# Kernel optimization log

Measured on AMD Instinct MI355X. Metric: run time of the kernel, lower is better.

The kernel has to match this reference:

```python
import jax, jax.numpy as jnp
import numpy as np

PAD = 4          # displacement radius
WIN = 2 * PAD + 1  # 9 -> 81 displacement channels


def setup_inputs() -> dict:
    key = jax.random.key(0)
    k1, k2 = jax.random.split(key)
    B, C, H, W = 4, 128, 128, 256
    first = jax.random.normal(k1, (B, C, H, W), dtype=jnp.float32)
    second = jax.random.normal(k2, (B, C, H, W), dtype=jnp.float32)
    return {"first": first, "second": second}


def reference(first, second):
    """FlowNet-style correlation / cost volume.

    out[b, (p+4)*9 + (o+4), y, x] = mean_c first[b,c,y,x] * second_pad[b,c,y+p+4,x+o+4]
    with second zero-padded by 4 on each spatial side.
    """
    B, C, H, W = first.shape
    second_pad = jnp.pad(second, ((0, 0), (0, 0), (PAD, PAD), (PAD, PAD)))
    outs = []
    for p in range(WIN):        # vertical displacement index (p - 4)
        for o in range(WIN):    # horizontal displacement index (o - 4)
            shifted = second_pad[:, :, p:p + H, o:o + W]  # [B,C,H,W]
            outs.append(jnp.mean(first * shifted, axis=1))  # [B,H,W]
    return jnp.stack(outs, axis=1)  # [B,81,H,W]
```

## Files before the change

### kernel.cpp

```cpp
#include <hip/hip_runtime.h>
#include <hip/hip_bf16.h>


namespace {
constexpr int kC = 128, kH = 128, kW = 256;
constexpr int kWin = 9;
constexpr int kYB = 4, kXB = 16;
constexpr int kSR = kYB + 8;
constexpr int kSX = kXB + 16;
constexpr int kCP = 40;
constexpr int kKC = 32;
constexpr int kNK = kC / kKC;
constexpr int kSSz = kSR * kSX * kCP;
constexpr int kFSz = kYB * kXB * kCP;
constexpr int kBuf = kSSz + kFSz;
constexpr int kSU = kSR * (kSX / 4) * (kKC / 8);
constexpr int kFU = kYB * (kXB / 4) * (kKC / 8);
constexpr int kTU = kSU + kFU;
constexpr int kThreads = 512;
constexpr int kBlocks = 4 * (kH / kYB) * (kW / kXB);
constexpr int kOS = kYB * kXB + 4;
constexpr int kCStr = kH * kW;

typedef __attribute__((ext_vector_type(8))) short bf16x8;
typedef __attribute__((ext_vector_type(4))) float f32x4;
}

__global__ __launch_bounds__(kThreads, 4) void corr_mfma(
    const float* __restrict__ first,
    const float* __restrict__ second,
    float* __restrict__ out)
{
    __shared__ __align__(16) unsigned short lds[2 * kBuf];

    const int tid  = threadIdx.x;
    const int lane = tid & 63;
    const int wid  = tid >> 6;
    const int yslot = wid >> 1;
    const int Ns    = wid & 1;

    const int bid = blockIdx.x;
    const int xcd = bid & 7;
    const int seq = bid >> 3;
    const int xt  = seq & 15;
    const int g   = ((seq >> 4) << 3) + xcd;
    const int b   = g >> 5;
    const int y0  = (g & 31) * kYB;
    const int X0  = xt * kXB;

    const size_t ibase = (size_t)b * kC * kCStr;

    const float* ug = nullptr;
    int ul = -1;
    if (tid < kSU) {
        int co = tid & 3, xq = (tid >> 2) & 7, row = tid >> 5;
        int yg = y0 - 4 + row, xg = X0 - 8 + xq * 4;
        ul = (row * kSX + xq * 4) * kCP + co * 8;
        if (yg >= 0 && yg < kH && xg >= 0 && xg <= kW - 4)
            ug = second + ibase + (size_t)(co * 8) * kCStr + (size_t)yg * kW + xg;
    } else if (tid < kTU) {
        int u2 = tid - kSU;
        int co = u2 & 3, xq = (u2 >> 2) & 3, row = u2 >> 4;
        ul = kSSz + (row * kXB + xq * 4) * kCP + co * 8;
        ug = first + ibase + (size_t)(co * 8) * kCStr
                   + (size_t)(y0 + row) * kW + (X0 + xq * 4);
    }

    float4 pvA[8], pvB[8];
    auto issue = [&](float4* pv, int kc) {
        if (ul < 0) return;
        const float4 z = make_float4(0.f, 0.f, 0.f, 0.f);
#pragma unroll
        for (int j = 0; j < 8; ++j) pv[j] = z;
        if (ug) {
            const float* gp = ug + (size_t)kc * kKC * kCStr;
#pragma unroll
            for (int j = 0; j < 8; ++j)
                pv[j] = *(const float4*)(gp + (size_t)j * kCStr);
        }
    };
    auto write_lds = [&](int base, const float4* pv) {
        if (ul < 0) return;
#pragma unroll
        for (int xi = 0; xi < 4; ++xi) {
            union { uint4 q; __hip_bfloat162 h[4]; } pk;
#pragma unroll
            for (int jj = 0; jj < 4; ++jj) {
                float lo = ((const float*)&pv[2 * jj])[xi];
                float hi = ((const float*)&pv[2 * jj + 1])[xi];
                pk.h[jj] = __float22bfloat162_rn(make_float2(lo, hi));
            }
            *(uint4*)&lds[base + ul + xi * kCP] = pk.q;
        }
    };

    const int l15 = lane & 15, lg = lane >> 4;
    const int aoff = kSSz + (yslot * kXB + l15) * kCP + lg * 8;
    const int boff = (yslot * kSX + Ns * 16 + l15) * kCP + lg * 8;

    f32x4 acc[kWin];
    {
        f32x4 z = {0.f, 0.f, 0.f, 0.f};
#pragma unroll
        for (int p = 0; p < kWin; ++p) acc[p] = z;
    }

    auto compute = [&](int base) {
        bf16x8 a = *(const bf16x8*)&lds[base + aoff];
#pragma unroll
        for (int p = 0; p < kWin; ++p) {
            bf16x8 bb = *(const bf16x8*)&lds[base + boff + p * (kSX * kCP)];
            acc[p] = __builtin_amdgcn_mfma_f32_16x16x32_bf16(a, bb, acc[p], 0, 0, 0);
        }
    };

    issue(pvA, 0);
    issue(pvB, 1);
    write_lds(0, pvA);
    __syncthreads();
    issue(pvA, 2);
    compute(0);
    write_lds(kBuf, pvB);
    __syncthreads();
    issue(pvB, 3);
    compute(kBuf);
    write_lds(0, pvA);
    __syncthreads();
    compute(0);
    write_lds(kBuf, pvB);
    __syncthreads();
    compute(kBuf);

    float* outb = (float*)lds;
    const float inv = 1.0f / (float)kC;
    const int delta = Ns ? 12 : -4;
#pragma unroll
    for (int p = 0; p < kWin; ++p)
#pragma unroll
        for (int r = 0; r < 4; ++r) {
            int m = (lg << 2) + r;
            int o = l15 - m + delta;
            if (o >= 0 && o < kWin) {
                int d = p * kWin + o;
                outb[d * kOS + yslot * kXB + m] = acc[p][r] * inv;
            }
        }
    __syncthreads();

    const size_t ob = (size_t)b * (kWin * kWin) * kCStr;
    for (int i = tid; i < kWin * kWin * kYB * (kXB / 4); i += kThreads) {
        int d  = i >> 4;
        int r2 = i & 15;
        int yy = r2 >> 2, xq = r2 & 3;
        float4 v = *(const float4*)&outb[d * kOS + yy * kXB + xq * 4];
        *(float4*)&out[ob + ((size_t)d * kH + (y0 + yy)) * kW + X0 + xq * 4] = v;
    }
}

extern "C" void kernel_launch(void* const* d_in, const int* in_sizes, int n_in,
                              void* d_out, int out_size, void* d_ws, size_t ws_size,
                              hipStream_t stream) {
    const float* first  = (const float*)d_in[0];
    const float* second = (const float*)d_in[1];
    float* out = (float*)d_out;
    dim3 grid(kBlocks);
    dim3 block(kThreads);
    hipLaunchKernelGGL(corr_mfma, grid, block, 0, stream, first, second, out);
}
```

Before: 65.89 us.

## Make blocks persistent over four x-tiles with prefetch of next tile

Each block now handles four consecutive x-tiles in a loop, so the grid is cut by four. The first two channel chunks of the next tile are prefetched into registers while the current tile finishes its last compute and output store. This is meant to hide global load latency across tiles and amortise block launch cost. The price is fewer blocks for latency hiding, extra barriers per tile, and no reuse of the overlapping second-tensor halo between adjacent tiles.

```diff
diff --git a/kernel.cpp b/kernel.cpp
--- a/kernel.cpp
+++ b/kernel.cpp
@@ -10,7 +10,6 @@
 constexpr int kSX = kXB + 16;
 constexpr int kCP = 40;
 constexpr int kKC = 32;
-constexpr int kNK = kC / kKC;
 constexpr int kSSz = kSR * kSX * kCP;
 constexpr int kFSz = kYB * kXB * kCP;
 constexpr int kBuf = kSSz + kFSz;
@@ -18,7 +17,8 @@
 constexpr int kFU = kYB * (kXB / 4) * (kKC / 8);
 constexpr int kTU = kSU + kFU;
 constexpr int kThreads = 512;
-constexpr int kBlocks = 4 * (kH / kYB) * (kW / kXB);
+constexpr int kTiles = 4;
+constexpr int kBlocks = 4 * (kH / kYB) * (kW / (kXB * kTiles));
 constexpr int kOS = kYB * kXB + 4;
 constexpr int kCStr = kH * kW;
 
@@ -42,32 +42,42 @@
     const int bid = blockIdx.x;
     const int xcd = bid & 7;
     const int seq = bid >> 3;
-    const int xt  = seq & 15;
-    const int g   = ((seq >> 4) << 3) + xcd;
-    const int b   = g >> 5;
-    const int y0  = (g & 31) * kYB;
-    const int X0  = xt * kXB;
+    const int xg  = seq & 3;
+    const int gg  = ((seq >> 2) << 3) + xcd;
+    const int b   = gg >> 5;
+    const int y0  = (gg & 31) * kYB;
+    const int X0base = xg * (kXB * kTiles);
 
     const size_t ibase = (size_t)b * kC * kCStr;
 
-    const float* ug = nullptr;
     int ul = -1;
     if (tid < kSU) {
         int co = tid & 3, xq = (tid >> 2) & 7, row = tid >> 5;
-        int yg = y0 - 4 + row, xg = X0 - 8 + xq * 4;
         ul = (row * kSX + xq * 4) * kCP + co * 8;
-        if (yg >= 0 && yg < kH && xg >= 0 && xg <= kW - 4)
-            ug = second + ibase + (size_t)(co * 8) * kCStr + (size_t)yg * kW + xg;
     } else if (tid < kTU) {
         int u2 = tid - kSU;
         int co = u2 & 3, xq = (u2 >> 2) & 3, row = u2 >> 4;
         ul = kSSz + (row * kXB + xq * 4) * kCP + co * 8;
-        ug = first + ibase + (size_t)(co * 8) * kCStr
-                   + (size_t)(y0 + row) * kW + (X0 + xq * 4);
     }
+    auto make_ug = [&](int X0) -> const float* {
+        if (tid < kSU) {
+            int co = tid & 3, xq = (tid >> 2) & 7, row = tid >> 5;
+            int yg = y0 - 4 + row, gx = X0 - 8 + xq * 4;
+            if (yg >= 0 && yg < kH && gx >= 0 && gx <= kW - 4)
+                return second + ibase + (size_t)(co * 8) * kCStr
+                              + (size_t)yg * kW + gx;
+            return nullptr;
+        } else if (tid < kTU) {
+            int u2 = tid - kSU;
+            int co = u2 & 3, xq = (u2 >> 2) & 3, row = u2 >> 4;
+            return first + ibase + (size_t)(co * 8) * kCStr
+                         + (size_t)(y0 + row) * kW + (X0 + xq * 4);
+        }
+        return nullptr;
+    };
 
     float4 pvA[8], pvB[8];
-    auto issue = [&](float4* pv, int kc) {
+    auto issue = [&](float4* pv, const float* ug, int kc) {
         if (ul < 0) return;
         const float4 z = make_float4(0.f, 0.f, 0.f, 0.f);
 #pragma unroll
@@ -99,12 +109,6 @@
     const int boff = (yslot * kSX + Ns * 16 + l15) * kCP + lg * 8;
 
     f32x4 acc[kWin];
-    {
-        f32x4 z = {0.f, 0.f, 0.f, 0.f};
-#pragma unroll
-        for (int p = 0; p < kWin; ++p) acc[p] = z;
-    }
-
     auto compute = [&](int base) {
         bf16x8 a = *(const bf16x8*)&lds[base + aoff];
 #pragma unroll
@@ -114,46 +118,64 @@
         }
     };
 
-    issue(pvA, 0);
-    issue(pvB, 1);
-    write_lds(0, pvA);
-    __syncthreads();
-    issue(pvA, 2);
-    compute(0);
-    write_lds(kBuf, pvB);
-    __syncthreads();
-    issue(pvB, 3);
-    compute(kBuf);
-    write_lds(0, pvA);
-    __syncthreads();
-    compute(0);
-    write_lds(kBuf, pvB);
-    __syncthreads();
-    compute(kBuf);
-
     float* outb = (float*)lds;
     const float inv = 1.0f / (float)kC;
     const int delta = Ns ? 12 : -4;
+    const size_t ob = (size_t)b * (kWin * kWin) * kCStr;
+
+    const float* ugT = make_ug(X0base);
+    issue(pvA, ugT, 0);
+    issue(pvB, ugT, 1);
+
+#pragma unroll 1
+    for (int t = 0; t < kTiles; ++t) {
+        const int X0 = X0base + t * kXB;
+        {
+            f32x4 z = {0.f, 0.f, 0.f, 0.f};
 #pragma unroll
-    for (int p = 0; p < kWin; ++p)
+            for (int p = 0; p < kWin; ++p) acc[p] = z;
+        }
+        write_lds(0, pvA);
+        issue(pvA, ugT, 2);
+        __syncthreads();
+        compute(0);
+        write_lds(kBuf, pvB);
+        issue(pvB, ugT, 3);
+        __syncthreads();
+        compute(kBuf);
+        write_lds(0, pvA);
+        __syncthreads();
+        compute(0);
+        write_lds(kBuf, pvB);
+        if (t < kTiles - 1) {
+            ugT = make_ug(X0 + kXB);
+            issue(pvA, ugT, 0);
+            issue(pvB, ugT, 1);
+        }
+        __syncthreads();
+        compute(kBuf);
+        __syncthreads();
+
 #pragma unroll
-        for (int r = 0; r < 4; ++r) {
-            int m = (lg << 2) + r;
-            int o = l15 - m + delta;
-            if (o >= 0 && o < kWin) {
-                int d = p * kWin + o;
-                outb[d * kOS + yslot * kXB + m] = acc[p][r] * inv;
+        for (int p = 0; p < kWin; ++p)
+#pragma unroll
+            for (int r = 0; r < 4; ++r) {
+                int m = (lg << 2) + r;
+                int o = l15 - m + delta;
+                if (o >= 0 && o < kWin) {
+                    int d = p * kWin + o;
+                    outb[d * kOS + yslot * kXB + m] = acc[p][r] * inv;
+                }
             }
+        __syncthreads();
+        for (int i = tid; i < kWin * kWin * kYB * (kXB / 4); i += kThreads) {
+            int d  = i >> 4;
+            int r2 = i & 15;
+            int yy = r2 >> 2, xq = r2 & 3;
+            float4 v = *(const float4*)&outb[d * kOS + yy * kXB + xq * 4];
+            *(float4*)&out[ob + ((size_t)d * kH + (y0 + yy)) * kW + X0 + xq * 4] = v;
         }
-    __syncthreads();
-
-    const size_t ob = (size_t)b * (kWin * kWin) * kCStr;
-    for (int i = tid; i < kWin * kWin * kYB * (kXB / 4); i += kThreads) {
-        int d  = i >> 4;
-        int r2 = i & 15;
-        int yy = r2 >> 2, xq = r2 & 3;
-        float4 v = *(const float4*)&outb[d * kOS + yy * kXB + xq * 4];
-        *(float4*)&out[ob + ((size_t)d * kH + (y0 + yy)) * kW + X0 + xq * 4] = v;
+        __syncthreads();
     }
 }
 
```

Result: slower. 163.4 us (+148.0%).
